# Performance work log

Measured on AMD Instinct MI355X. Metric: run time of the kernel, lower is better.

## Reference

```python
import jax, jax.numpy as jnp
import numpy as np

K = 16          # max_points
S = 3           # num_scales
DM = 256        # d_model
KD = 16         # k_dim geometric projection
TAU = 1e-4
LN_EPS = 1e-5


def _boundaries():
    edges = [(i, j) for i in range(K) for j in range(i + 1, K)]
    tris = [(i, j, k) for i in range(K) for j in range(i + 1, K) for k in range(j + 1, K)]
    E, T = len(edges), len(tris)
    B1 = np.zeros((K, E), np.float32)
    for e, (i, j) in enumerate(edges):
        B1[i, e] = -1.0
        B1[j, e] = 1.0
    eidx = {e: n for n, e in enumerate(edges)}
    B2 = np.zeros((E, T), np.float32)
    for t, (i, j, k) in enumerate(tris):
        B2[eidx[(j, k)], t] = 1.0
        B2[eidx[(i, k)], t] = -1.0
        B2[eidx[(i, j)], t] = 1.0
    ei = np.array([e[0] for e in edges])
    ej = np.array([e[1] for e in edges])
    tij = np.array([eidx[(a, b)] for a, b, c in tris])
    tjk = np.array([eidx[(b, c)] for a, b, c in tris])
    tik = np.array([eidx[(a, c)] for a, b, c in tris])
    return (jnp.asarray(B1), jnp.asarray(B2), jnp.asarray(np.abs(B1)),
            jnp.asarray(ei), jnp.asarray(ej), jnp.asarray(tij), jnp.asarray(tjk), jnp.asarray(tik))

_B1, _B2, _ABS, _EI, _EJ, _TIJ, _TJK, _TIK = _boundaries()
E = _B1.shape[1]  # 120


def _ln(x, g, b):
    m = jnp.mean(x, -1, keepdims=True)
    v = jnp.mean((x - m) ** 2, -1, keepdims=True)
    return (x - m) * jax.lax.rsqrt(v + LN_EPS) * g + b


def setup_inputs() -> dict:
    key = jax.random.key(0)
    ks = jax.random.split(key, 12)
    B = 1024
    p = lambda k, *sh: 0.02 * jax.random.normal(k, sh, dtype=jnp.float32)
    return {
        'x': jax.random.normal(ks[0], (B, K, DM), dtype=jnp.float32),
        'mask': jnp.ones((B, K), dtype=jnp.float32),
        'Wg': p(ks[1], DM, KD), 'bg': jnp.zeros((KD,), jnp.float32),
        'log_scales': jnp.linspace(-1.5, 1.5, S, dtype=jnp.float32),
        'Wv': p(ks[2], DM, DM * S), 'bv': jnp.zeros((DM * S,), jnp.float32),
        'We': p(ks[3], DM, DM * S), 'be': jnp.zeros((DM * S,), jnp.float32),
        'Wo': p(ks[4], DM * S * 2, DM), 'bo': jnp.zeros((DM,), jnp.float32),
        'ln1_g': jnp.ones((DM,), jnp.float32), 'ln1_b': jnp.zeros((DM,), jnp.float32),
        'ln2_g': jnp.ones((DM,), jnp.float32), 'ln2_b': jnp.zeros((DM,), jnp.float32),
        'Wf1': p(ks[5], DM, DM * 4), 'bf1': jnp.zeros((DM * 4,), jnp.float32),
        'Wf2': p(ks[6], DM * 4, DM), 'bf2': jnp.zeros((DM,), jnp.float32),
    }


def reference(x, mask, Wg, bg, log_scales, Wv, bv, We, be, Wo, bo,
              ln1_g, ln1_b, ln2_g, ln2_b, Wf1, bf1, Wf2, bf2):
    B = x.shape[0]
    xn = _ln(x, ln1_g, ln1_b)
    P = xn @ Wg + bg                                   # [B,K,KD]
    m2 = mask[:, :, None] * mask[:, None, :]           # [B,K,K]
    p2 = jnp.sum(P * P, -1)
    Dsq = jnp.maximum(p2[:, :, None] + p2[:, None, :] - 2.0 * jnp.einsum('bkc,blc->bkl', P, P), 0.0) * m2
    sig2 = jnp.exp(log_scales) ** 2                    # [S]
    V0 = (xn @ Wv + bv).reshape(B, K, S, DM).transpose(0, 2, 1, 3)   # [B,S,K,D]
    Eraw = jnp.einsum('ke,bkd->bed', _ABS, xn)         # [B,E,D]
    Ein = (Eraw @ We + be).reshape(B, E, S, DM).transpose(0, 2, 1, 3)  # [B,S,E,D]
    aff = jnp.exp(-Dsq[:, None] / (2.0 * sig2[None, :, None, None] + 1e-8)) * m2[:, None]  # [B,S,K,K]
    W1 = aff[:, :, _EI, _EJ]                           # [B,S,E]
    W2 = W1[:, :, _TIJ] * W1[:, :, _TJK] * W1[:, :, _TIK]  # [B,S,T]
    L0 = jnp.einsum('ke,bse,le->bskl', _B1, W1, _B1) + TAU * jnp.eye(K, dtype=x.dtype)
    node_upd = jnp.einsum('bskl,bsld->bskd', L0, V0)
    term_down = jnp.einsum('ke,bk,kf->bef', _B1, mask, _B1)
    term_up = jnp.einsum('et,bst,ft->bsef', _B2, W2, _B2)
    L1 = term_down[:, None] + term_up + TAU * jnp.eye(E, dtype=x.dtype)
    edge_msg = jnp.einsum('bsef,bsfd->bsed', L1, Ein)
    edge_upd = jnp.einsum('ke,bsed->bskd', _ABS, edge_msg)
    nu = node_upd.transpose(0, 2, 1, 3).reshape(B, K, S * DM)
    eu = edge_upd.transpose(0, 2, 1, 3).reshape(B, K, S * DM)
    x = x + (jnp.concatenate([nu, eu], -1) @ Wo + bo)  # residual + attn_out (dropout=eval noop)
    h = _ln(x, ln2_g, ln2_b)
    return x + (jax.nn.gelu(h @ Wf1 + bf1, approximate=False) @ Wf2 + bf2)
```

## Files before the change

kernel.cpp:

```cpp
#include <hip/hip_runtime.h>
#include <hip/hip_bf16.h>
#include <cstdint>
#include <cstddef>

#define TAU 1e-4f
#define LN_EPS 1e-5f

typedef unsigned short ushort_t;
typedef unsigned int uint_t;
typedef __attribute__((ext_vector_type(8))) short short8;
typedef __attribute__((ext_vector_type(4))) float f32x4;

__device__ __forceinline__ ushort_t f2bf(float f) {
    union { float f; unsigned int u; } c; c.f = f;
    unsigned int r = (c.u + 0x7fffu + ((c.u >> 16) & 1u)) >> 16;
    return (ushort_t)r;
}
__device__ __forceinline__ void glds16(const void* g, void* l) {
    __builtin_amdgcn_global_load_lds((const __attribute__((address_space(1))) unsigned int*)g,
                                     (__attribute__((address_space(3))) unsigned int*)l,
                                     16, 0, 0);
}

__global__ __launch_bounds__(256) void kA(
    const float* __restrict__ xg, const float* __restrict__ maskg,
    const float* __restrict__ Wg, const float* __restrict__ bg,
    const float* __restrict__ ls, const float* __restrict__ g1,
    const float* __restrict__ b1, ushort_t* __restrict__ Mcat,
    float* __restrict__ gbuf,
    const float* __restrict__ Wv, const float* __restrict__ We,
    const float* __restrict__ Wo, const float* __restrict__ bv,
    const float* __restrict__ be, const float* __restrict__ Wf1,
    const float* __restrict__ Wf2, ushort_t* __restrict__ WcatT,
    ushort_t* __restrict__ Wf1T, ushort_t* __restrict__ Wf2T,
    float* __restrict__ cvpart, float* __restrict__ beWo) {
    __shared__ __align__(16) float POOL[9872];
    const int tid = threadIdx.x;

    if (blockIdx.x >= 1024) {
        const int id = blockIdx.x - 1024;
        if (id < 384) {
            float (*rowS)[256] = (float(*)[256])POOL;
            const int q0 = (id & 63) * 4;
            const int w = id >> 6;
            const int half = w / 3, s = w - half * 3;
            const float* src = half ? We : Wv;
#pragma unroll
            for (int r = 0; r < 4; ++r)
                rowS[r][tid] = src[(size_t)(q0 + r) * 768 + s * 256 + tid];
            __syncthreads();
            const float* wo = Wo + (size_t)(half * 768 + s * 256) * 256 + tid;
            float a0 = 0.f, a1 = 0.f, a2 = 0.f, a3 = 0.f;
            for (int d = 0; d < 256; ++d) {
                float wv = wo[(size_t)d * 256];
                a0 += rowS[0][d] * wv; a1 += rowS[1][d] * wv;
                a2 += rowS[2][d] * wv; a3 += rowS[3][d] * wv;
            }
            const int rt = half * 3 + s;
            ushort4 pk;
            pk.x = f2bf(a0); pk.y = f2bf(a1); pk.z = f2bf(a2); pk.w = f2bf(a3);
            *(ushort4*)&WcatT[(size_t)tid * 1536 + rt * 256 + q0] = pk;
        } else if (id < 390) {
            const int w = id - 384;
            const int half = w / 3, s = w - half * 3;
            const float* vec = half ? be : bv;
            POOL[tid] = vec[s * 256 + tid];
            __syncthreads();
            const float* wo = Wo + (size_t)(half * 768 + s * 256) * 256 + tid;
            float acc = 0.f;
            for (int d = 0; d < 256; ++d) acc += POOL[d] * wo[(size_t)d * 256];
            if (half) beWo[s * 256 + tid] = acc;
            else cvpart[s * 256 + tid] = acc;
        } else {
            float (*tS)[65] = (float(*)[65])POOL;
            const float* src; ushort_t* dst;
            int sr0, sc0, ss, dr0, dc0, ds_;
            if (id < 454) {
                int t = id - 390; int ki = t & 3, ni = t >> 2;
                src = Wf1; ss = 1024; sr0 = ki * 64; sc0 = ni * 64;
                dst = Wf1T; ds_ = 256; dr0 = ni * 64; dc0 = ki * 64;
            } else {
                int t = id - 454; int ki = t >> 2, ni = t & 3;
                src = Wf2; ss = 256; sr0 = ki * 64; sc0 = ni * 64;
                dst = Wf2T; ds_ = 1024; dr0 = ni * 64; dc0 = ki * 64;
            }
            const int rl = tid >> 6, cl = tid & 63;
#pragma unroll
            for (int p = 0; p < 16; ++p) {
                int r = p * 4 + rl;
                tS[r][cl] = src[(size_t)(sr0 + r) * ss + sc0 + cl];
            }
            __syncthreads();
#pragma unroll
            for (int p = 0; p < 16; ++p) {
                int r = p * 4 + rl;
                dst[(size_t)(dr0 + r) * ds_ + dc0 + cl] = f2bf(tS[cl][r]);
            }
        }
        return;
    }

    const int b = blockIdx.x;
    float (*XS)[260] = (float(*)[260])POOL;
    float* WB = POOL + 4160;
    float (*Pl)[17] = (float(*)[17])(POOL + 8320);
    float (*dotm)[17] = (float(*)[17])(POOL + 8592);
    float* Ms = POOL + 8320;
    float* mk = POOL + 9856;
    float (*WgT)[260] = (float(*)[260])WB;
    float (*DsqS)[17] = (float(*)[17])WB;
    float (*Wh)[16][17] = (float(*)[16][17])(WB + 272);
    float* Ts = WB + 1088;

    const float* xb = xg + (size_t)b * 4096;
#pragma unroll
    for (int i = 0; i < 4; ++i) {
        int idx = tid * 4 + i * 1024;
        int k = idx >> 8, c = idx & 255;
        float4 v = *(const float4*)&xb[idx];
        XS[k][c] = v.x; XS[k][c + 1] = v.y; XS[k][c + 2] = v.z; XS[k][c + 3] = v.w;
    }
    {
        const float4* wgp = (const float4*)(Wg + tid * 16);
        float4 w0 = wgp[0], w1 = wgp[1], w2 = wgp[2], w3 = wgp[3];
        WgT[0][tid] = w0.x; WgT[1][tid] = w0.y; WgT[2][tid] = w0.z; WgT[3][tid] = w0.w;
        WgT[4][tid] = w1.x; WgT[5][tid] = w1.y; WgT[6][tid] = w1.z; WgT[7][tid] = w1.w;
        WgT[8][tid] = w2.x; WgT[9][tid] = w2.y; WgT[10][tid] = w2.z; WgT[11][tid] = w2.w;
        WgT[12][tid] = w3.x; WgT[13][tid] = w3.y; WgT[14][tid] = w3.z; WgT[15][tid] = w3.w;
    }
    if (tid < 16) mk[tid] = maskg[b * 16 + tid];
    __syncthreads();

    {
        const int k = tid >> 4, c = tid & 15;
        float s = 0.f;
#pragma unroll
        for (int j = 0; j < 16; ++j) s += XS[k][c + 16 * j];
        for (int off = 8; off; off >>= 1) s += __shfl_down(s, off, 16);
        float mean = __shfl(s, 0, 16) * (1.f / 256.f);
        float vs = 0.f;
#pragma unroll
        for (int j = 0; j < 16; ++j) { float d = XS[k][c + 16 * j] - mean; vs += d * d; }
        for (int off = 8; off; off >>= 1) vs += __shfl_down(vs, off, 16);
        float rstd = rsqrtf(__shfl(vs, 0, 16) * (1.f / 256.f) + LN_EPS);
#pragma unroll
        for (int j = 0; j < 16; ++j) {
            int cc = c + 16 * j;
            XS[k][cc] = (XS[k][cc] - mean) * rstd * g1[cc] + b1[cc];
        }
    }
    __syncthreads();

    {
        const int k = tid >> 4, c = tid & 15;
        float acc = bg[c];
#pragma unroll
        for (int q4 = 0; q4 < 64; ++q4) {
            float4 wv = *(const float4*)&WgT[c][q4 * 4];
            float4 xv = *(const float4*)&XS[k][q4 * 4];
            acc += wv.x * xv.x + wv.y * xv.y + wv.z * xv.z + wv.w * xv.w;
        }
        Pl[k][c] = acc;
    }
    __syncthreads();
    const int k = tid >> 4, m = tid & 15;
    {
        float d = 0.f;
#pragma unroll
        for (int c = 0; c < 16; ++c) d += Pl[k][c] * Pl[m][c];
        dotm[k][m] = d;
    }
    __syncthreads();
    {
        float v = dotm[k][k] + dotm[m][m] - 2.f * dotm[k][m];
        DsqS[k][m] = fmaxf(v, 0.f) * mk[k] * mk[m];
    }
    {
        float d = DsqS[k][m];
        float mm = mk[k] * mk[m];
#pragma unroll
        for (int s = 0; s < 3; ++s) {
            float i2 = 1.f / (2.f * expf(2.f * ls[s]) + 1e-8f);
            Wh[s][k][m] = (k == m) ? 0.f : expf(-d * i2) * mm;
        }
    }
    __syncthreads();
    if (tid < 48) {
        int s = tid >> 4, j = tid & 15;
        float t = 0.f;
        for (int i = 0; i < j; ++i) {
            float d = 0.f;
            for (int jj = j + 1; jj < 16; ++jj) d += Wh[s][j][jj] * Wh[s][i][jj];
            t += Wh[s][i][j] * d;
        }
        Ts[s * 16 + j] = t;
    }
    __syncthreads();
    float gd = 0.f;
#pragma unroll
    for (int o = 0; o < 16; ++o) {
        if (o == m) continue;
        int u = o < m ? o : m, v = o < m ? m : o;
        float gu = (u == k) ? (float)(2 * k - 15) : ((u > k) ? 1.f : -1.f);
        float gv = (v == k) ? (float)(2 * k - 15) : ((v > k) ? 1.f : -1.f);
        gd += -gu * mk[u] + gv * mk[v];
        if (u == k || v == k) gd += TAU;
    }
#pragma unroll
    for (int s = 0; s < 3; ++s) {
        float rs = 0.f;
#pragma unroll
        for (int o = 0; o < 16; ++o) rs += Wh[s][k][o];
        float l0 = (k == m) ? (rs + TAU) : -Wh[s][k][m];
        float G = gd + ((k == m) ? 4.f * Ts[s * 16 + k] : 0.f);
        Ms[s * 256 + tid] = l0;
        Ms[768 + s * 256 + tid] = G;
        float gg = G;
        for (int off = 8; off; off >>= 1) gg += __shfl_down(gg, off, 16);
        if (m == 0) gbuf[b * 48 + k * 3 + s] = 0.5f * gg;
    }
    __syncthreads();

    {
        const int q2 = (tid & 127) * 2;
        const int rtbase = (tid >> 7) * 3;
        float xv0[16], xv1[16];
#pragma unroll
        for (int l = 0; l < 16; ++l) { xv0[l] = XS[l][q2]; xv1[l] = XS[l][q2 + 1]; }
        const size_t obase = (size_t)b * 16 * 1536;
#pragma unroll
        for (int rtt = 0; rtt < 3; ++rtt) {
            const int rt = rtbase + rtt;
#pragma unroll
            for (int kk = 0; kk < 16; ++kk) {
                const float4* mp = (const float4*)&Ms[rt * 256 + kk * 16];
                float4 m0 = mp[0], m1 = mp[1], m2 = mp[2], m3 = mp[3];
                float a0 = m0.x * xv0[0] + m0.y * xv0[1] + m0.z * xv0[2] + m0.w * xv0[3]
                         + m1.x * xv0[4] + m1.y * xv0[5] + m1.z * xv0[6] + m1.w * xv0[7]
                         + m2.x * xv0[8] + m2.y * xv0[9] + m2.z * xv0[10] + m2.w * xv0[11]
                         + m3.x * xv0[12] + m3.y * xv0[13] + m3.z * xv0[14] + m3.w * xv0[15];
                float a1 = m0.x * xv1[0] + m0.y * xv1[1] + m0.z * xv1[2] + m0.w * xv1[3]
                         + m1.x * xv1[4] + m1.y * xv1[5] + m1.z * xv1[6] + m1.w * xv1[7]
                         + m2.x * xv1[8] + m2.y * xv1[9] + m2.z * xv1[10] + m2.w * xv1[11]
                         + m3.x * xv1[12] + m3.y * xv1[13] + m3.z * xv1[14] + m3.w * xv1[15];
                uint_t pk = (uint_t)f2bf(a0) | ((uint_t)f2bf(a1) << 16);
                *(uint_t*)&Mcat[obase + (size_t)kk * 1536 + rt * 256 + q2] = pk;
            }
        }
    }
}

__device__ __forceinline__ void gemm128(const ushort_t* __restrict__ A,
                                        const ushort_t* __restrict__ Bt,
                                        int Kdim, int m0, int n0,
                                        f32x4 acc[4][4],
                                        ushort_t (*As)[32], ushort_t (*Bs)[32]) {
    const int tid = threadIdx.x;
    const int wave = tid >> 6, lane = tid & 63;
    const int lq = lane >> 4, lr = lane & 15;
    const int wm = wave >> 1, wn = wave & 1;
    const int r = tid >> 2, ca = (tid & 3) << 3;
    const ushort_t* Ag0 = A + (size_t)(m0 + r) * Kdim + ca;
    const ushort_t* Ag1 = A + (size_t)(m0 + 64 + r) * Kdim + ca;
    const ushort_t* Bg0 = Bt + (size_t)(n0 + r) * Kdim + ca;
    const ushort_t* Bg1 = Bt + (size_t)(n0 + 64 + r) * Kdim + ca;
    char* AsD0 = (char*)As + wave * 1024;
    char* AsD1 = (char*)As + 4096 + wave * 1024;
    char* BsD0 = (char*)Bs + wave * 1024;
    char* BsD1 = (char*)Bs + 4096 + wave * 1024;
    for (int kt = 0; kt < Kdim; kt += 32) {
        __syncthreads();
        glds16(Ag0 + kt, AsD0);
        glds16(Ag1 + kt, AsD1);
        glds16(Bg0 + kt, BsD0);
        glds16(Bg1 + kt, BsD1);
        __syncthreads();
        short8 af[4], bfr[4];
#pragma unroll
        for (int i = 0; i < 4; ++i) af[i] = *(const short8*)&As[wm * 64 + i * 16 + lr][lq * 8];
#pragma unroll
        for (int j = 0; j < 4; ++j) bfr[j] = *(const short8*)&Bs[wn * 64 + j * 16 + lr][lq * 8];
#pragma unroll
        for (int i = 0; i < 4; ++i)
#pragma unroll
            for (int j = 0; j < 4; ++j)
                acc[i][j] = __builtin_amdgcn_mfma_f32_16x16x32_bf16(af[i], bfr[j], acc[i][j], 0, 0, 0);
    }
}

__device__ __forceinline__ void gemm64(const ushort_t* __restrict__ A,
                                       const ushort_t* __restrict__ Bt,
                                       int Kdim, int m0, int n0,
                                       f32x4 acc[2][4],
                                       ushort_t (*As)[32], ushort_t (*Bs)[32]) {
    const int tid = threadIdx.x;
    const int wave = tid >> 6, lane = tid & 63;
    const int lq = lane >> 4, lr = lane & 15;
    const int wm = wave >> 1, wn = wave & 1;
    const int r = tid >> 2, ca = (tid & 3) << 3;
    const ushort_t* Ag = A + (size_t)(m0 + r) * Kdim + ca;
    const ushort_t* Bg0 = Bt + (size_t)(n0 + r) * Kdim + ca;
    const ushort_t* Bg1 = Bt + (size_t)(n0 + 64 + r) * Kdim + ca;
    char* AsD = (char*)As + wave * 1024;
    char* Bs0D = (char*)Bs + wave * 1024;
    char* Bs1D = (char*)Bs + 4096 + wave * 1024;
    for (int kt = 0; kt < Kdim; kt += 32) {
        __syncthreads();
        glds16(Ag + kt, AsD);
        glds16(Bg0 + kt, Bs0D);
        glds16(Bg1 + kt, Bs1D);
        __syncthreads();
        short8 af[2], bfr[4];
#pragma unroll
        for (int i = 0; i < 2; ++i) af[i] = *(const short8*)&As[wm * 32 + i * 16 + lr][lq * 8];
#pragma unroll
        for (int j = 0; j < 4; ++j) bfr[j] = *(const short8*)&Bs[wn * 64 + j * 16 + lr][lq * 8];
#pragma unroll
        for (int i = 0; i < 2; ++i)
#pragma unroll
            for (int j = 0; j < 4; ++j)
                acc[i][j] = __builtin_amdgcn_mfma_f32_16x16x32_bf16(af[i], bfr[j], acc[i][j], 0, 0, 0);
    }
}

__global__ __launch_bounds__(256) void kZY_gemm(
    const ushort_t* __restrict__ Mcat, const ushort_t* __restrict__ WcatT,
    const float* __restrict__ xin, const float* __restrict__ bo,
    const float* __restrict__ cvpart, const float* __restrict__ beWo,
    const float* __restrict__ gbuf, float* __restrict__ xp) {
    __shared__ ushort_t As[64][32];
    __shared__ ushort_t Bs[128][32];
    __shared__ float cvS[128], bewS[3][128], gblk[64][3];
    const int tid = threadIdx.x;
    const int m0 = blockIdx.x * 64, n0 = blockIdx.y * 128;
    if (tid < 128) {
        int n = n0 + tid;
        cvS[tid] = bo[n] + TAU * (cvpart[n] + cvpart[256 + n] + cvpart[512 + n]);
        bewS[0][tid] = beWo[n];
        bewS[1][tid] = beWo[256 + n];
        bewS[2][tid] = beWo[512 + n];
    }
    if (tid < 192) { int rr = tid / 3, s = tid - rr * 3; gblk[rr][s] = gbuf[(size_t)(m0 + rr) * 3 + s]; }
    f32x4 acc[2][4] = {};
    gemm64(Mcat, WcatT, 1536, m0, n0, acc, As, Bs);
    const int wave = tid >> 6, lane = tid & 63, lq = lane >> 4, lr = lane & 15;
    const int wm = wave >> 1, wn = wave & 1;
#pragma unroll
    for (int i = 0; i < 2; ++i)
#pragma unroll
        for (int j = 0; j < 4; ++j) {
            int nl = wn * 64 + j * 16 + lr;
#pragma unroll
            for (int v = 0; v < 4; ++v) {
                int rl = wm * 32 + i * 16 + lq * 4 + v;
                size_t idx = (size_t)(m0 + rl) * 256 + n0 + nl;
                xp[idx] = acc[i][j][v] + xin[idx] + cvS[nl] +
                          gblk[rl][0] * bewS[0][nl] + gblk[rl][1] * bewS[1][nl] +
                          gblk[rl][2] * bewS[2][nl];
            }
        }
}

__global__ __launch_bounds__(256) void k_ln2(const float* __restrict__ xp,
                                             const float* __restrict__ g2,
                                             const float* __restrict__ b2,
                                             ushort_t* __restrict__ h) {
    const int tid = threadIdx.x;
    const int row = blockIdx.x * 4 + (tid >> 6);
    const int lane = tid & 63;
    const float* xr = xp + (size_t)row * 256;
    float v0 = xr[lane], v1 = xr[lane + 64], v2 = xr[lane + 128], v3 = xr[lane + 192];
    float s = v0 + v1 + v2 + v3;
    for (int m = 32; m; m >>= 1) s += __shfl_xor(s, m, 64);
    float mean = s * (1.f / 256.f);
    float d0 = v0 - mean, d1 = v1 - mean, d2 = v2 - mean, d3 = v3 - mean;
    float q = d0 * d0 + d1 * d1 + d2 * d2 + d3 * d3;
    for (int m = 32; m; m >>= 1) q += __shfl_xor(q, m, 64);
    float rstd = rsqrtf(q * (1.f / 256.f) + LN_EPS);
    ushort_t* hr = h + (size_t)row * 256;
    hr[lane] = f2bf(d0 * rstd * g2[lane] + b2[lane]);
    hr[lane + 64] = f2bf(d1 * rstd * g2[lane + 64] + b2[lane + 64]);
    hr[lane + 128] = f2bf(d2 * rstd * g2[lane + 128] + b2[lane + 128]);
    hr[lane + 192] = f2bf(d3 * rstd * g2[lane + 192] + b2[lane + 192]);
}

__global__ __launch_bounds__(256) void k3_gemm(const ushort_t* __restrict__ h,
                                               const ushort_t* __restrict__ Wf1T,
                                               const float* __restrict__ bf1,
                                               ushort_t* __restrict__ F1g) {
    __shared__ ushort_t As[128][32];
    __shared__ ushort_t Bs[128][32];
    const int tid = threadIdx.x;
    const int m0 = blockIdx.x * 128, n0 = blockIdx.y * 128;
    f32x4 acc[4][4] = {};
    gemm128(h, Wf1T, 256, m0, n0, acc, As, Bs);
    const int wave = tid >> 6, lane = tid & 63, lq = lane >> 4, lr = lane & 15;
    const int wm = wave >> 1, wn = wave & 1;
#pragma unroll
    for (int i = 0; i < 4; ++i)
#pragma unroll
        for (int j = 0; j < 4; ++j) {
            int n = n0 + wn * 64 + j * 16 + lr;
            float bn = bf1[n];
#pragma unroll
            for (int v = 0; v < 4; ++v) {
                int rg = m0 + wm * 64 + i * 16 + lq * 4 + v;
                float u = acc[i][j][v] + bn;
                float gl = 0.5f * u * (1.f + erff(u * 0.70710678118f));
                F1g[(size_t)rg * 1024 + n] = f2bf(gl);
            }
        }
}

__global__ __launch_bounds__(256) void k4_gemm(const ushort_t* __restrict__ F1g,
                                               const ushort_t* __restrict__ Wf2T,
                                               const float* __restrict__ bf2,
                                               const float* __restrict__ xp,
                                               float* __restrict__ out) {
    __shared__ ushort_t As[64][32];
    __shared__ ushort_t Bs[128][32];
    const int tid = threadIdx.x;
    const int m0 = blockIdx.x * 64, n0 = blockIdx.y * 128;
    f32x4 acc[2][4] = {};
    gemm64(F1g, Wf2T, 1024, m0, n0, acc, As, Bs);
    const int wave = tid >> 6, lane = tid & 63, lq = lane >> 4, lr = lane & 15;
    const int wm = wave >> 1, wn = wave & 1;
#pragma unroll
    for (int i = 0; i < 2; ++i)
#pragma unroll
        for (int j = 0; j < 4; ++j) {
            int n = n0 + wn * 64 + j * 16 + lr;
            float bn = bf2[n];
#pragma unroll
            for (int v = 0; v < 4; ++v) {
                size_t idx = (size_t)(m0 + wm * 32 + i * 16 + lq * 4 + v) * 256 + n;
                out[idx] = xp[idx] + acc[i][j][v] + bn;
            }
        }
}

extern "C" void kernel_launch(void* const* d_in, const int* in_sizes, int n_in,
                              void* d_out, int out_size, void* d_ws, size_t ws_size,
                              hipStream_t stream) {
    const float* x = (const float*)d_in[0];
    const float* mask = (const float*)d_in[1];
    const float* Wg = (const float*)d_in[2];
    const float* bg = (const float*)d_in[3];
    const float* ls = (const float*)d_in[4];
    const float* Wv = (const float*)d_in[5];
    const float* bv = (const float*)d_in[6];
    const float* We = (const float*)d_in[7];
    const float* be = (const float*)d_in[8];
    const float* Wo = (const float*)d_in[9];
    const float* bo = (const float*)d_in[10];
    const float* g1 = (const float*)d_in[11];
    const float* b1 = (const float*)d_in[12];
    const float* g2 = (const float*)d_in[13];
    const float* b2 = (const float*)d_in[14];
    const float* Wf1 = (const float*)d_in[15];
    const float* bf1 = (const float*)d_in[16];
    const float* Wf2 = (const float*)d_in[17];
    const float* bf2 = (const float*)d_in[18];
    float* out = (float*)d_out;

    char* ws = (char*)d_ws;
    ushort_t* Mcat = (ushort_t*)(ws);
    ushort_t* F1g = (ushort_t*)(ws);
    ushort_t* WcatT = (ushort_t*)(ws + 50331648);
    ushort_t* Wf1T = (ushort_t*)(ws + 51118080);
    ushort_t* Wf2T = (ushort_t*)(ws + 51642368);
    float* cvpart = (float*)(ws + 52166656);
    float* beWo = (float*)(ws + 52169728);
    float* gbuf = (float*)(ws + 52172800);
    float* xp = (float*)(ws + 52369408);
    ushort_t* h = (ushort_t*)(ws + 69146624);

    kA<<<dim3(1542), dim3(256), 0, stream>>>(x, mask, Wg, bg, ls, g1, b1,
                                             Mcat, gbuf,
                                             Wv, We, Wo, bv, be, Wf1, Wf2,
                                             WcatT, Wf1T, Wf2T, cvpart, beWo);
    kZY_gemm<<<dim3(256, 2), dim3(256), 0, stream>>>(Mcat, WcatT, x, bo, cvpart, beWo, gbuf, xp);
    k_ln2<<<dim3(4096), dim3(256), 0, stream>>>(xp, g2, b2, h);
    k3_gemm<<<dim3(128, 8), dim3(256), 0, stream>>>(h, Wf1T, bf1, F1g);
    k4_gemm<<<dim3(256, 2), dim3(256), 0, stream>>>(F1g, Wf2T, bf2, xp, out);
}
```

Before: 219.0 us.

## Double-buffer LDS tiles in GEMM kernels and shrink k3 M-tile to 64

Replaces the single-buffered GEMM mainloops with double-buffered versions. Each version issues the next K-slice's global-to-LDS loads before computing on the current slice, and uses explicit vmcnt waits and barriers in place of two __syncthreads per step. k3_gemm also switches from 128x128 tiles to 64x128 tiles, doubling its grid. The goal is to hide global load latency behind MFMA work. The cost is twice the LDS per block and hand-written waitcnt logic that depends on ordering being correct.

```diff
diff --git a/kernel.cpp b/kernel.cpp
--- a/kernel.cpp
+++ b/kernel.cpp
@@ -250,11 +250,81 @@
     }
 }
 
-__device__ __forceinline__ void gemm128(const ushort_t* __restrict__ A,
-                                        const ushort_t* __restrict__ Bt,
-                                        int Kdim, int m0, int n0,
-                                        f32x4 acc[4][4],
-                                        ushort_t (*As)[32], ushort_t (*Bs)[32]) {
+__device__ __forceinline__ void gemm64_db(
+    const ushort_t* __restrict__ A, const ushort_t* __restrict__ Bt,
+    int Kdim, int m0, int n0, f32x4 acc[2][4],
+    ushort_t (*As0)[32], ushort_t (*As1)[32],
+    ushort_t (*Bs0)[32], ushort_t (*Bs1)[32]) {
+    const int tid = threadIdx.x;
+    const int wave = tid >> 6, lane = tid & 63;
+    const int lq = lane >> 4, lr = lane & 15;
+    const int wm = wave >> 1, wn = wave & 1;
+    const int r = tid >> 2, ca = (tid & 3) << 3;
+    const ushort_t* Ag  = A  + (size_t)(m0 + r) * Kdim + ca;
+    const ushort_t* Bg0 = Bt + (size_t)(n0 + r) * Kdim + ca;
+    const ushort_t* Bg1 = Bt + (size_t)(n0 + 64 + r) * Kdim + ca;
+    char* aD0  = (char*)As0 + wave * 1024;
+    char* aD1  = (char*)As1 + wave * 1024;
+    char* b0D0 = (char*)Bs0 + wave * 1024;
+    char* b0D1 = (char*)Bs0 + 4096 + wave * 1024;
+    char* b1D0 = (char*)Bs1 + wave * 1024;
+    char* b1D1 = (char*)Bs1 + 4096 + wave * 1024;
+
+    glds16(Ag, aD0); glds16(Bg0, b0D0); glds16(Bg1, b0D1);
+
+    for (int kt = 0; kt < Kdim; kt += 64) {
+        {
+            const int kn = kt + 32;
+            if (kn < Kdim) {
+                glds16(Ag + kn, aD1); glds16(Bg0 + kn, b1D0); glds16(Bg1 + kn, b1D1);
+                asm volatile("s_waitcnt vmcnt(3)" ::: "memory");
+            } else {
+                asm volatile("s_waitcnt vmcnt(0)" ::: "memory");
+            }
+            __builtin_amdgcn_s_barrier();
+            short8 af[2], bfr[4];
+#pragma unroll
+            for (int i = 0; i < 2; ++i) af[i] = *(const short8*)&As0[wm * 32 + i * 16 + lr][lq * 8];
+#pragma unroll
+            for (int j = 0; j < 4; ++j) bfr[j] = *(const short8*)&Bs0[wn * 64 + j * 16 + lr][lq * 8];
+#pragma unroll
+            for (int i = 0; i < 2; ++i)
+#pragma unroll
+                for (int j = 0; j < 4; ++j)
+                    acc[i][j] = __builtin_amdgcn_mfma_f32_16x16x32_bf16(af[i], bfr[j], acc[i][j], 0, 0, 0);
+            asm volatile("s_waitcnt lgkmcnt(0)" ::: "memory");
+            __builtin_amdgcn_s_barrier();
+        }
+        {
+            const int kn = kt + 64;
+            if (kn < Kdim) {
+                glds16(Ag + kn, aD0); glds16(Bg0 + kn, b0D0); glds16(Bg1 + kn, b0D1);
+                asm volatile("s_waitcnt vmcnt(3)" ::: "memory");
+            } else {
+                asm volatile("s_waitcnt vmcnt(0)" ::: "memory");
+            }
+            __builtin_amdgcn_s_barrier();
+            short8 af[2], bfr[4];
+#pragma unroll
+            for (int i = 0; i < 2; ++i) af[i] = *(const short8*)&As1[wm * 32 + i * 16 + lr][lq * 8];
+#pragma unroll
+            for (int j = 0; j < 4; ++j) bfr[j] = *(const short8*)&Bs1[wn * 64 + j * 16 + lr][lq * 8];
+#pragma unroll
+            for (int i = 0; i < 2; ++i)
+#pragma unroll
+                for (int j = 0; j < 4; ++j)
+                    acc[i][j] = __builtin_amdgcn_mfma_f32_16x16x32_bf16(af[i], bfr[j], acc[i][j], 0, 0, 0);
+            asm volatile("s_waitcnt lgkmcnt(0)" ::: "memory");
+            __builtin_amdgcn_s_barrier();
+        }
+    }
+}
+
+__device__ __forceinline__ void gemm128_db(
+    const ushort_t* __restrict__ A, const ushort_t* __restrict__ Bt,
+    int Kdim, int m0, int n0, f32x4 acc[4][4],
+    ushort_t (*As0)[32], ushort_t (*As1)[32],
+    ushort_t (*Bs0)[32], ushort_t (*Bs1)[32]) {
     const int tid = threadIdx.x;
     const int wave = tid >> 6, lane = tid & 63;
     const int lq = lane >> 4, lr = lane & 15;
@@ -264,62 +334,64 @@
     const ushort_t* Ag1 = A + (size_t)(m0 + 64 + r) * Kdim + ca;
     const ushort_t* Bg0 = Bt + (size_t)(n0 + r) * Kdim + ca;
     const ushort_t* Bg1 = Bt + (size_t)(n0 + 64 + r) * Kdim + ca;
-    char* AsD0 = (char*)As + wave * 1024;
-    char* AsD1 = (char*)As + 4096 + wave * 1024;
-    char* BsD0 = (char*)Bs + wave * 1024;
-    char* BsD1 = (char*)Bs + 4096 + wave * 1024;
-    for (int kt = 0; kt < Kdim; kt += 32) {
-        __syncthreads();
-        glds16(Ag0 + kt, AsD0);
-        glds16(Ag1 + kt, AsD1);
-        glds16(Bg0 + kt, BsD0);
-        glds16(Bg1 + kt, BsD1);
-        __syncthreads();
-        short8 af[4], bfr[4];
-#pragma unroll
-        for (int i = 0; i < 4; ++i) af[i] = *(const short8*)&As[wm * 64 + i * 16 + lr][lq * 8];
-#pragma unroll
-        for (int j = 0; j < 4; ++j) bfr[j] = *(const short8*)&Bs[wn * 64 + j * 16 + lr][lq * 8];
-#pragma unroll
-        for (int i = 0; i < 4; ++i)
-#pragma unroll
-            for (int j = 0; j < 4; ++j)
-                acc[i][j] = __builtin_amdgcn_mfma_f32_16x16x32_bf16(af[i], bfr[j], acc[i][j], 0, 0, 0);
-    }
-}
-
-__device__ __forceinline__ void gemm64(const ushort_t* __restrict__ A,
-                                       const ushort_t* __restrict__ Bt,
-                                       int Kdim, int m0, int n0,
-                                       f32x4 acc[2][4],
-                                       ushort_t (*As)[32], ushort_t (*Bs)[32]) {
-    const int tid = threadIdx.x;
-    const int wave = tid >> 6, lane = tid & 63;
-    const int lq = lane >> 4, lr = lane & 15;
-    const int wm = wave >> 1, wn = wave & 1;
-    const int r = tid >> 2, ca = (tid & 3) << 3;
-    const ushort_t* Ag = A + (size_t)(m0 + r) * Kdim + ca;
-    const ushort_t* Bg0 = Bt + (size_t)(n0 + r) * Kdim + ca;
-    const ushort_t* Bg1 = Bt + (size_t)(n0 + 64 + r) * Kdim + ca;
-    char* AsD = (char*)As + wave * 1024;
-    char* Bs0D = (char*)Bs + wave * 1024;
-    char* Bs1D = (char*)Bs + 4096 + wave * 1024;
-    for (int kt = 0; kt < Kdim; kt += 32) {
-        __syncthreads();
-        glds16(Ag + kt, AsD);
-        glds16(Bg0 + kt, Bs0D);
-        glds16(Bg1 + kt, Bs1D);
-        __syncthreads();
-        short8 af[2], bfr[4];
-#pragma unroll
-        for (int i = 0; i < 2; ++i) af[i] = *(const short8*)&As[wm * 32 + i * 16 + lr][lq * 8];
-#pragma unroll
-        for (int j = 0; j < 4; ++j) bfr[j] = *(const short8*)&Bs[wn * 64 + j * 16 + lr][lq * 8];
-#pragma unroll
-        for (int i = 0; i < 2; ++i)
-#pragma unroll
-            for (int j = 0; j < 4; ++j)
-                acc[i][j] = __builtin_amdgcn_mfma_f32_16x16x32_bf16(af[i], bfr[j], acc[i][j], 0, 0, 0);
+    char* a0D0 = (char*)As0 + wave * 1024;
+    char* a0D1 = (char*)As0 + 4096 + wave * 1024;
+    char* a1D0 = (char*)As1 + wave * 1024;
+    char* a1D1 = (char*)As1 + 4096 + wave * 1024;
+    char* b0D0 = (char*)Bs0 + wave * 1024;
+    char* b0D1 = (char*)Bs0 + 4096 + wave * 1024;
+    char* b1D0 = (char*)Bs1 + wave * 1024;
+    char* b1D1 = (char*)Bs1 + 4096 + wave * 1024;
+
+    glds16(Ag0, a0D0); glds16(Ag1, a0D1); glds16(Bg0, b0D0); glds16(Bg1, b0D1);
+
+    for (int kt = 0; kt < Kdim; kt += 64) {
+        {
+            const int kn = kt + 32;
+            if (kn < Kdim) {
+                glds16(Ag0 + kn, a1D0); glds16(Ag1 + kn, a1D1);
+                glds16(Bg0 + kn, b1D0); glds16(Bg1 + kn, b1D1);
+                asm volatile("s_waitcnt vmcnt(4)" ::: "memory");
+            } else {
+                asm volatile("s_waitcnt vmcnt(0)" ::: "memory");
+            }
+            __builtin_amdgcn_s_barrier();
+            short8 af[4], bfr[4];
+#pragma unroll
+            for (int i = 0; i < 4; ++i) af[i] = *(const short8*)&As0[wm * 64 + i * 16 + lr][lq * 8];
+#pragma unroll
+            for (int j = 0; j < 4; ++j) bfr[j] = *(const short8*)&Bs0[wn * 64 + j * 16 + lr][lq * 8];
+#pragma unroll
+            for (int i = 0; i < 4; ++i)
+#pragma unroll
+                for (int j = 0; j < 4; ++j)
+                    acc[i][j] = __builtin_amdgcn_mfma_f32_16x16x32_bf16(af[i], bfr[j], acc[i][j], 0, 0, 0);
+            asm volatile("s_waitcnt lgkmcnt(0)" ::: "memory");
+            __builtin_amdgcn_s_barrier();
+        }
+        {
+            const int kn = kt + 64;
+            if (kn < Kdim) {
+                glds16(Ag0 + kn, a0D0); glds16(Ag1 + kn, a0D1);
+                glds16(Bg0 + kn, b0D0); glds16(Bg1 + kn, b0D1);
+                asm volatile("s_waitcnt vmcnt(4)" ::: "memory");
+            } else {
+                asm volatile("s_waitcnt vmcnt(0)" ::: "memory");
+            }
+            __builtin_amdgcn_s_barrier();
+            short8 af[4], bfr[4];
+#pragma unroll
+            for (int i = 0; i < 4; ++i) af[i] = *(const short8*)&As1[wm * 64 + i * 16 + lr][lq * 8];
+#pragma unroll
+            for (int j = 0; j < 4; ++j) bfr[j] = *(const short8*)&Bs1[wn * 64 + j * 16 + lr][lq * 8];
+#pragma unroll
+            for (int i = 0; i < 4; ++i)
+#pragma unroll
+                for (int j = 0; j < 4; ++j)
+                    acc[i][j] = __builtin_amdgcn_mfma_f32_16x16x32_bf16(af[i], bfr[j], acc[i][j], 0, 0, 0);
+            asm volatile("s_waitcnt lgkmcnt(0)" ::: "memory");
+            __builtin_amdgcn_s_barrier();
+        }
     }
 }
 
@@ -328,8 +400,8 @@
     const float* __restrict__ xin, const float* __restrict__ bo,
     const float* __restrict__ cvpart, const float* __restrict__ beWo,
     const float* __restrict__ gbuf, float* __restrict__ xp) {
-    __shared__ ushort_t As[64][32];
-    __shared__ ushort_t Bs[128][32];
+    __shared__ ushort_t As0[64][32], As1[64][32];
+    __shared__ ushort_t Bs0[128][32], Bs1[128][32];
     __shared__ float cvS[128], bewS[3][128], gblk[64][3];
     const int tid = threadIdx.x;
     const int m0 = blockIdx.x * 64, n0 = blockIdx.y * 128;
@@ -342,7 +414,7 @@
     }
     if (tid < 192) { int rr = tid / 3, s = tid - rr * 3; gblk[rr][s] = gbuf[(size_t)(m0 + rr) * 3 + s]; }
     f32x4 acc[2][4] = {};
-    gemm64(Mcat, WcatT, 1536, m0, n0, acc, As, Bs);
+    gemm64_db(Mcat, WcatT, 1536, m0, n0, acc, As0, As1, Bs0, Bs1);
     const int wave = tid >> 6, lane = tid & 63, lq = lane >> 4, lr = lane & 15;
     const int wm = wave >> 1, wn = wave & 1;
 #pragma unroll
@@ -388,23 +460,23 @@
                                                const ushort_t* __restrict__ Wf1T,
                                                const float* __restrict__ bf1,
                                                ushort_t* __restrict__ F1g) {
-    __shared__ ushort_t As[128][32];
-    __shared__ ushort_t Bs[128][32];
-    const int tid = threadIdx.x;
-    const int m0 = blockIdx.x * 128, n0 = blockIdx.y * 128;
-    f32x4 acc[4][4] = {};
-    gemm128(h, Wf1T, 256, m0, n0, acc, As, Bs);
+    __shared__ ushort_t As0[64][32], As1[64][32];
+    __shared__ ushort_t Bs0[128][32], Bs1[128][32];
+    const int tid = threadIdx.x;
+    const int m0 = blockIdx.x * 64, n0 = blockIdx.y * 128;
+    f32x4 acc[2][4] = {};
+    gemm64_db(h, Wf1T, 256, m0, n0, acc, As0, As1, Bs0, Bs1);
     const int wave = tid >> 6, lane = tid & 63, lq = lane >> 4, lr = lane & 15;
     const int wm = wave >> 1, wn = wave & 1;
 #pragma unroll
-    for (int i = 0; i < 4; ++i)
+    for (int i = 0; i < 2; ++i)
 #pragma unroll
         for (int j = 0; j < 4; ++j) {
             int n = n0 + wn * 64 + j * 16 + lr;
             float bn = bf1[n];
 #pragma unroll
             for (int v = 0; v < 4; ++v) {
-                int rg = m0 + wm * 64 + i * 16 + lq * 4 + v;
+                int rg = m0 + wm * 32 + i * 16 + lq * 4 + v;
                 float u = acc[i][j][v] + bn;
                 float gl = 0.5f * u * (1.f + erff(u * 0.70710678118f));
                 F1g[(size_t)rg * 1024 + n] = f2bf(gl);
@@ -417,12 +489,12 @@
                                                const float* __restrict__ bf2,
                                                const float* __restrict__ xp,
                                                float* __restrict__ out) {
-    __shared__ ushort_t As[64][32];
-    __shared__ ushort_t Bs[128][32];
+    __shared__ ushort_t As0[64][32], As1[64][32];
+    __shared__ ushort_t Bs0[128][32], Bs1[128][32];
     const int tid = threadIdx.x;
     const int m0 = blockIdx.x * 64, n0 = blockIdx.y * 128;
     f32x4 acc[2][4] = {};
-    gemm64(F1g, Wf2T, 1024, m0, n0, acc, As, Bs);
+    gemm64_db(F1g, Wf2T, 1024, m0, n0, acc, As0, As1, Bs0, Bs1);
     const int wave = tid >> 6, lane = tid & 63, lq = lane >> 4, lr = lane & 15;
     const int wm = wave >> 1, wn = wave & 1;
 #pragma unroll
@@ -481,6 +553,6 @@
                                              WcatT, Wf1T, Wf2T, cvpart, beWo);
     kZY_gemm<<<dim3(256, 2), dim3(256), 0, stream>>>(Mcat, WcatT, x, bo, cvpart, beWo, gbuf, xp);
     k_ln2<<<dim3(4096), dim3(256), 0, stream>>>(xp, g2, b2, h);
-    k3_gemm<<<dim3(128, 8), dim3(256), 0, stream>>>(h, Wf1T, bf1, F1g);
+    k3_gemm<<<dim3(256, 8), dim3(256), 0, stream>>>(h, Wf1T, bf1, F1g);
     k4_gemm<<<dim3(256, 2), dim3(256), 0, stream>>>(F1g, Wf2T, bf2, xp, out);
 }
```

Result: faster. 205.4 us (-6.2%).

## Triple-buffer GEMM LDS loads with async prefetch and shrink FFN1 tiles

Applied to the files above, without the earlier changes.

Replaces the two synchronous GEMM helpers with a single triple-buffered routine. It issues global-to-LDS loads two k-tiles ahead and uses vmcnt waits and raw barriers, so memory latency overlaps with the MFMA work. The FFN1 GEMM switches from 128x128 to 64x128 tiles with twice as many blocks, which raises parallelism at the cost of reloading B tiles more often. The triple buffers triple LDS use per block, which may lower occupancy.

```diff
diff --git a/kernel.cpp b/kernel.cpp
--- a/kernel.cpp
+++ b/kernel.cpp
@@ -250,76 +250,62 @@
     }
 }
 
-__device__ __forceinline__ void gemm128(const ushort_t* __restrict__ A,
-                                        const ushort_t* __restrict__ Bt,
-                                        int Kdim, int m0, int n0,
-                                        f32x4 acc[4][4],
-                                        ushort_t (*As)[32], ushort_t (*Bs)[32]) {
+__device__ __forceinline__ void gemm64_tb(
+    const ushort_t* __restrict__ A, const ushort_t* __restrict__ Bt,
+    int Kdim, int m0, int n0, f32x4 acc[2][4],
+    ushort_t (*AsB)[64][32], ushort_t (*BsB)[128][32]) {
     const int tid = threadIdx.x;
     const int wave = tid >> 6, lane = tid & 63;
     const int lq = lane >> 4, lr = lane & 15;
     const int wm = wave >> 1, wn = wave & 1;
     const int r = tid >> 2, ca = (tid & 3) << 3;
-    const ushort_t* Ag0 = A + (size_t)(m0 + r) * Kdim + ca;
-    const ushort_t* Ag1 = A + (size_t)(m0 + 64 + r) * Kdim + ca;
+    const ushort_t* Ag  = A  + (size_t)(m0 + r) * Kdim + ca;
     const ushort_t* Bg0 = Bt + (size_t)(n0 + r) * Kdim + ca;
     const ushort_t* Bg1 = Bt + (size_t)(n0 + 64 + r) * Kdim + ca;
-    char* AsD0 = (char*)As + wave * 1024;
-    char* AsD1 = (char*)As + 4096 + wave * 1024;
-    char* BsD0 = (char*)Bs + wave * 1024;
-    char* BsD1 = (char*)Bs + 4096 + wave * 1024;
-    for (int kt = 0; kt < Kdim; kt += 32) {
-        __syncthreads();
-        glds16(Ag0 + kt, AsD0);
-        glds16(Ag1 + kt, AsD1);
-        glds16(Bg0 + kt, BsD0);
-        glds16(Bg1 + kt, BsD1);
-        __syncthreads();
-        short8 af[4], bfr[4];
-#pragma unroll
-        for (int i = 0; i < 4; ++i) af[i] = *(const short8*)&As[wm * 64 + i * 16 + lr][lq * 8];
-#pragma unroll
-        for (int j = 0; j < 4; ++j) bfr[j] = *(const short8*)&Bs[wn * 64 + j * 16 + lr][lq * 8];
-#pragma unroll
-        for (int i = 0; i < 4; ++i)
+    const int NT = Kdim >> 5;
+    char* aD0  = (char*)AsB[0] + wave * 1024;
+    char* aD1  = (char*)AsB[1] + wave * 1024;
+    char* aD2  = (char*)AsB[2] + wave * 1024;
+    char* b0D0 = (char*)BsB[0] + wave * 1024;
+    char* b0D1 = (char*)BsB[1] + wave * 1024;
+    char* b0D2 = (char*)BsB[2] + wave * 1024;
+    char* b1D0 = (char*)BsB[0] + 4096 + wave * 1024;
+    char* b1D1 = (char*)BsB[1] + 4096 + wave * 1024;
+    char* b1D2 = (char*)BsB[2] + 4096 + wave * 1024;
+
+    glds16(Ag, aD0);      glds16(Bg0, b0D0);      glds16(Bg1, b1D0);
+    glds16(Ag + 32, aD1); glds16(Bg0 + 32, b0D1); glds16(Bg1 + 32, b1D1);
+
+    int bc = 0;
+    for (int t = 0; t < NT; ++t) {
+        const int t2 = t + 2;
+        if (t2 < NT) {
+            char* aT  = (bc == 0) ? aD2  : ((bc == 1) ? aD0  : aD1);
+            char* b0T = (bc == 0) ? b0D2 : ((bc == 1) ? b0D0 : b0D1);
+            char* b1T = (bc == 0) ? b1D2 : ((bc == 1) ? b1D0 : b1D1);
+            glds16(Ag + t2 * 32, aT);
+            glds16(Bg0 + t2 * 32, b0T);
+            glds16(Bg1 + t2 * 32, b1T);
+            asm volatile("s_waitcnt vmcnt(6)" ::: "memory");
+        } else if (t + 1 < NT) {
+            asm volatile("s_waitcnt vmcnt(3)" ::: "memory");
+        } else {
+            asm volatile("s_waitcnt vmcnt(0)" ::: "memory");
+        }
+        __builtin_amdgcn_s_barrier();
+        short8 af[2], bfr[4];
+#pragma unroll
+        for (int i = 0; i < 2; ++i) af[i] = *(const short8*)&AsB[bc][wm * 32 + i * 16 + lr][lq * 8];
+#pragma unroll
+        for (int j = 0; j < 4; ++j) bfr[j] = *(const short8*)&BsB[bc][wn * 64 + j * 16 + lr][lq * 8];
+#pragma unroll
+        for (int i = 0; i < 2; ++i)
 #pragma unroll
             for (int j = 0; j < 4; ++j)
                 acc[i][j] = __builtin_amdgcn_mfma_f32_16x16x32_bf16(af[i], bfr[j], acc[i][j], 0, 0, 0);
-    }
-}
-
-__device__ __forceinline__ void gemm64(const ushort_t* __restrict__ A,
-                                       const ushort_t* __restrict__ Bt,
-                                       int Kdim, int m0, int n0,
-                                       f32x4 acc[2][4],
-                                       ushort_t (*As)[32], ushort_t (*Bs)[32]) {
-    const int tid = threadIdx.x;
-    const int wave = tid >> 6, lane = tid & 63;
-    const int lq = lane >> 4, lr = lane & 15;
-    const int wm = wave >> 1, wn = wave & 1;
-    const int r = tid >> 2, ca = (tid & 3) << 3;
-    const ushort_t* Ag = A + (size_t)(m0 + r) * Kdim + ca;
-    const ushort_t* Bg0 = Bt + (size_t)(n0 + r) * Kdim + ca;
-    const ushort_t* Bg1 = Bt + (size_t)(n0 + 64 + r) * Kdim + ca;
-    char* AsD = (char*)As + wave * 1024;
-    char* Bs0D = (char*)Bs + wave * 1024;
-    char* Bs1D = (char*)Bs + 4096 + wave * 1024;
-    for (int kt = 0; kt < Kdim; kt += 32) {
-        __syncthreads();
-        glds16(Ag + kt, AsD);
-        glds16(Bg0 + kt, Bs0D);
-        glds16(Bg1 + kt, Bs1D);
-        __syncthreads();
-        short8 af[2], bfr[4];
-#pragma unroll
-        for (int i = 0; i < 2; ++i) af[i] = *(const short8*)&As[wm * 32 + i * 16 + lr][lq * 8];
-#pragma unroll
-        for (int j = 0; j < 4; ++j) bfr[j] = *(const short8*)&Bs[wn * 64 + j * 16 + lr][lq * 8];
-#pragma unroll
-        for (int i = 0; i < 2; ++i)
-#pragma unroll
-            for (int j = 0; j < 4; ++j)
-                acc[i][j] = __builtin_amdgcn_mfma_f32_16x16x32_bf16(af[i], bfr[j], acc[i][j], 0, 0, 0);
+        asm volatile("s_waitcnt lgkmcnt(0)" ::: "memory");
+        __builtin_amdgcn_s_barrier();
+        ++bc; if (bc >= 3) bc = 0;
     }
 }
 
@@ -328,8 +314,8 @@
     const float* __restrict__ xin, const float* __restrict__ bo,
     const float* __restrict__ cvpart, const float* __restrict__ beWo,
     const float* __restrict__ gbuf, float* __restrict__ xp) {
-    __shared__ ushort_t As[64][32];
-    __shared__ ushort_t Bs[128][32];
+    __shared__ ushort_t AsB[3][64][32];
+    __shared__ ushort_t BsB[3][128][32];
     __shared__ float cvS[128], bewS[3][128], gblk[64][3];
     const int tid = threadIdx.x;
     const int m0 = blockIdx.x * 64, n0 = blockIdx.y * 128;
@@ -342,7 +328,7 @@
     }
     if (tid < 192) { int rr = tid / 3, s = tid - rr * 3; gblk[rr][s] = gbuf[(size_t)(m0 + rr) * 3 + s]; }
     f32x4 acc[2][4] = {};
-    gemm64(Mcat, WcatT, 1536, m0, n0, acc, As, Bs);
+    gemm64_tb(Mcat, WcatT, 1536, m0, n0, acc, AsB, BsB);
     const int wave = tid >> 6, lane = tid & 63, lq = lane >> 4, lr = lane & 15;
     const int wm = wave >> 1, wn = wave & 1;
 #pragma unroll
@@ -388,23 +374,23 @@
                                                const ushort_t* __restrict__ Wf1T,
                                                const float* __restrict__ bf1,
                                                ushort_t* __restrict__ F1g) {
-    __shared__ ushort_t As[128][32];
-    __shared__ ushort_t Bs[128][32];
-    const int tid = threadIdx.x;
-    const int m0 = blockIdx.x * 128, n0 = blockIdx.y * 128;
-    f32x4 acc[4][4] = {};
-    gemm128(h, Wf1T, 256, m0, n0, acc, As, Bs);
+    __shared__ ushort_t AsB[3][64][32];
+    __shared__ ushort_t BsB[3][128][32];
+    const int tid = threadIdx.x;
+    const int m0 = blockIdx.x * 64, n0 = blockIdx.y * 128;
+    f32x4 acc[2][4] = {};
+    gemm64_tb(h, Wf1T, 256, m0, n0, acc, AsB, BsB);
     const int wave = tid >> 6, lane = tid & 63, lq = lane >> 4, lr = lane & 15;
     const int wm = wave >> 1, wn = wave & 1;
 #pragma unroll
-    for (int i = 0; i < 4; ++i)
+    for (int i = 0; i < 2; ++i)
 #pragma unroll
         for (int j = 0; j < 4; ++j) {
             int n = n0 + wn * 64 + j * 16 + lr;
             float bn = bf1[n];
 #pragma unroll
             for (int v = 0; v < 4; ++v) {
-                int rg = m0 + wm * 64 + i * 16 + lq * 4 + v;
+                int rg = m0 + wm * 32 + i * 16 + lq * 4 + v;
                 float u = acc[i][j][v] + bn;
                 float gl = 0.5f * u * (1.f + erff(u * 0.70710678118f));
                 F1g[(size_t)rg * 1024 + n] = f2bf(gl);
@@ -417,12 +403,12 @@
                                                const float* __restrict__ bf2,
                                                const float* __restrict__ xp,
                                                float* __restrict__ out) {
-    __shared__ ushort_t As[64][32];
-    __shared__ ushort_t Bs[128][32];
+    __shared__ ushort_t AsB[3][64][32];
+    __shared__ ushort_t BsB[3][128][32];
     const int tid = threadIdx.x;
     const int m0 = blockIdx.x * 64, n0 = blockIdx.y * 128;
     f32x4 acc[2][4] = {};
-    gemm64(F1g, Wf2T, 1024, m0, n0, acc, As, Bs);
+    gemm64_tb(F1g, Wf2T, 1024, m0, n0, acc, AsB, BsB);
     const int wave = tid >> 6, lane = tid & 63, lq = lane >> 4, lr = lane & 15;
     const int wm = wave >> 1, wn = wave & 1;
 #pragma unroll
@@ -481,6 +467,6 @@
                                              WcatT, Wf1T, Wf2T, cvpart, beWo);
     kZY_gemm<<<dim3(256, 2), dim3(256), 0, stream>>>(Mcat, WcatT, x, bo, cvpart, beWo, gbuf, xp);
     k_ln2<<<dim3(4096), dim3(256), 0, stream>>>(xp, g2, b2, h);
-    k3_gemm<<<dim3(128, 8), dim3(256), 0, stream>>>(h, Wf1T, bf1, F1g);
+    k3_gemm<<<dim3(256, 8), dim3(256), 0, stream>>>(h, Wf1T, bf1, F1g);
     k4_gemm<<<dim3(256, 2), dim3(256), 0, stream>>>(F1g, Wf2T, bf2, xp, out);
 }
```

Result: faster. 213.4 us (-2.6%).
